# Performance work log

Measured on AMD Instinct MI355X. Metric: run time of the kernel, lower is better.

## Reference

```python
import jax, jax.numpy as jnp
import numpy as np

GROUP_SIZE = 64  # matches init_kwargs group_size


def setup_inputs() -> dict:
    key = jax.random.key(0)
    k1, k2, k3, k4 = jax.random.split(key, 4)
    B, S, D_in, D_out = 4, 2048, 4096, 4096
    x = jax.random.normal(k1, (B, S, D_in), dtype=jnp.float32)
    # symmetric int8 quantized weights in [-127, 127]
    weight_quant = jax.random.randint(k2, (D_out, D_in), -127, 128, dtype=jnp.int32)
    num_groups = (D_out * D_in) // GROUP_SIZE
    # positive per-group scales (abs_max / 127 of a typical weight group)
    weight_scale = jax.random.uniform(k3, (num_groups,), dtype=jnp.float32,
                                      minval=1e-3, maxval=2e-2)
    bias = jax.random.normal(k4, (D_out,), dtype=jnp.float32) * 0.01
    return {"x": x, "weight_quant": weight_quant,
            "weight_scale": weight_scale, "bias": bias}


def reference(x, weight_quant, weight_scale, bias):
    # Group-wise symmetric dequantization: flatten row-major, scale each
    # contiguous group of GROUP_SIZE elements by its own scale.
    out_f, in_f = weight_quant.shape
    w = weight_quant.astype(jnp.float32).reshape(-1, GROUP_SIZE)  # [num_groups, G]
    w = w * weight_scale[:, None]
    w = w.reshape(out_f, in_f).astype(x.dtype)
    # F.linear(x, W, b) = x @ W^T + b
    return jnp.einsum('bsi,oi->bso', x, w) + bias
```

## Files before the change

### kernel.cpp

```cpp
#include <hip/hip_runtime.h>
#include <stdint.h>


#define BM 128
#define BN 128
#define BK 64

typedef __attribute__((ext_vector_type(8))) short short8;
typedef __attribute__((ext_vector_type(8))) unsigned short ushort8;
typedef __attribute__((ext_vector_type(16))) float f32x16;
typedef __attribute__((ext_vector_type(4))) float float4v;
typedef __attribute__((ext_vector_type(4))) int int4v;

typedef __attribute__((address_space(1))) void g_void;
typedef __attribute__((address_space(3))) void l_void;

__device__ __forceinline__ unsigned short f2bf(float f) {
  union { float f; unsigned int u; } v; v.f = f;
  unsigned int r = v.u + 0x7FFFu + ((v.u >> 16) & 1u);
  return (unsigned short)(r >> 16);
}

__device__ __forceinline__ void async_copy16(const void* g, void* l) {
  __builtin_amdgcn_global_load_lds((const g_void*)g, (l_void*)l, 16, 0, 0);
}

__global__ __launch_bounds__(256) void cvt_kernel(
    const float* __restrict__ x, const int* __restrict__ w,
    const float* __restrict__ s, unsigned short* __restrict__ ox,
    unsigned short* __restrict__ ow, int n8x, int n8w, int gx) {
  if ((int)blockIdx.x < gx) {
    int t = blockIdx.x * 256 + threadIdx.x;
    if (t >= n8x) return;
    const float4v* xp = (const float4v*)x + (size_t)t * 2;
    float4v a = xp[0], b = xp[1];
    ushort8 r;
    r[0] = f2bf(a[0]); r[1] = f2bf(a[1]); r[2] = f2bf(a[2]); r[3] = f2bf(a[3]);
    r[4] = f2bf(b[0]); r[5] = f2bf(b[1]); r[6] = f2bf(b[2]); r[7] = f2bf(b[3]);
    *(ushort8*)(ox + (size_t)t * 8) = r;
  } else {
    int t = ((int)blockIdx.x - gx) * 256 + threadIdx.x;
    if (t >= n8w) return;
    const int4v* wp = (const int4v*)w + (size_t)t * 2;
    int4v q0 = wp[0], q1 = wp[1];
    float sc = s[t >> 3];
    ushort8 r;
    r[0] = f2bf((float)q0[0] * sc); r[1] = f2bf((float)q0[1] * sc);
    r[2] = f2bf((float)q0[2] * sc); r[3] = f2bf((float)q0[3] * sc);
    r[4] = f2bf((float)q1[0] * sc); r[5] = f2bf((float)q1[1] * sc);
    r[6] = f2bf((float)q1[2] * sc); r[7] = f2bf((float)q1[3] * sc);
    *(ushort8*)(ow + (size_t)t * 8) = r;
  }
}

__global__ __launch_bounds__(256, 4) void gemm_pre(
    const unsigned short* __restrict__ Xb,
    const unsigned short* __restrict__ Wb,
    const float* __restrict__ bias,
    float* __restrict__ C, int M, int N, int K) {
  __shared__ unsigned char smem[(BM * BK + BN * BK) * 2];
  const int tid = threadIdx.x;
  const int lane = tid & 63, wid = tid >> 6;
  const int m0 = blockIdx.y * BM, n0 = blockIdx.x * BN;

  const int sr = lane >> 3;
  const int fc = (lane & 7) ^ sr;
  const int offA = ((m0 + wid * 32 + sr) * K + fc * 8) * 2;
  const int offB = ((n0 + wid * 32 + sr) * K + fc * 8) * 2;
  const char* Xc = (const char*)Xb;
  const char* Wc = (const char*)Wb;

  unsigned char* As = smem;
  unsigned char* Bs = smem + BM * BK * 2;
  unsigned char* ldsA = As + wid * 4096;
  unsigned char* ldsB = Bs + wid * 4096;

  const int l31 = lane & 31, lh = lane >> 5, le = lane & 7;
  const int wm = (wid & 1) * 64, wn = (wid >> 1) * 64;
  const unsigned char* Aw = As + (wm + l31) * 128;
  const unsigned char* Bw = Bs + (wn + l31) * 128;

  f32x16 acc[2][2];
#pragma unroll
  for (int i = 0; i < 2; i++)
#pragma unroll
    for (int j = 0; j < 2; j++) acc[i][j] = (f32x16)(0.f);

  for (int k0 = 0; k0 < K; k0 += BK) {
    const int kb = k0 * 2;
#pragma unroll
    for (int t = 0; t < 4; t++) {
      async_copy16(Xc + (size_t)(offA + kb) + (size_t)t * (K * 16), ldsA + t * 1024);
      async_copy16(Wc + (size_t)(offB + kb) + (size_t)t * (K * 16), ldsB + t * 1024);
    }
    __syncthreads();

#pragma unroll
    for (int s = 0; s < 4; s++) {
      const int off = ((s + 4 * lh) ^ le) << 4;
      short8 a0 = *(const short8*)(Aw + off);
      short8 a1 = *(const short8*)(Aw + 4096 + off);
      short8 b0 = *(const short8*)(Bw + off);
      short8 b1 = *(const short8*)(Bw + 4096 + off);
      acc[0][0] = __builtin_amdgcn_mfma_f32_32x32x16_bf16(a0, b0, acc[0][0], 0, 0, 0);
      acc[0][1] = __builtin_amdgcn_mfma_f32_32x32x16_bf16(a0, b1, acc[0][1], 0, 0, 0);
      acc[1][0] = __builtin_amdgcn_mfma_f32_32x32x16_bf16(a1, b0, acc[1][0], 0, 0, 0);
      acc[1][1] = __builtin_amdgcn_mfma_f32_32x32x16_bf16(a1, b1, acc[1][1], 0, 0, 0);
    }
    __syncthreads();
  }

  const int gm = m0 + wm + 4 * lh, gn = n0 + wn + l31;
#pragma unroll
  for (int j = 0; j < 2; j++) {
    const int col = gn + j * 32;
    const float bv = bias[col];
#pragma unroll
    for (int i = 0; i < 2; i++) {
      const int rbase = gm + i * 32;
      f32x16 v = acc[i][j];
#pragma unroll
      for (int r = 0; r < 16; r++) {
        const int row = rbase + (r & 3) + 8 * (r >> 2);
        C[(size_t)row * N + col] = v[r] + bv;
      }
    }
  }
}

__global__ __launch_bounds__(256) void gemm_fused(
    const float* __restrict__ Xf, const int* __restrict__ Wq,
    const float* __restrict__ Ws, const float* __restrict__ bias,
    float* __restrict__ C, int M, int N, int K) {
  __shared__ unsigned char smem[(BM * BK + BN * BK) * 2];
  const int tid = threadIdx.x;
  const int lane = tid & 63, wid = tid >> 6;
  const int m0 = blockIdx.y * BM, n0 = blockIdx.x * BN;
  const int sr = lane >> 3, fc = (lane & 7) ^ sr;
  const int arow = m0 + wid * 32 + sr, brow = n0 + wid * 32 + sr;
  unsigned char* As = smem;
  unsigned char* Bs = smem + BM * BK * 2;
  unsigned char* stA = As + wid * 4096 + lane * 16;
  unsigned char* stB = Bs + wid * 4096 + lane * 16;
  const int l31 = lane & 31, lh = lane >> 5, le = lane & 7;
  const int wm = (wid & 1) * 64, wn = (wid >> 1) * 64;
  const unsigned char* Aw = As + (wm + l31) * 128;
  const unsigned char* Bw = Bs + (wn + l31) * 128;
  const int Kg = K >> 6;

  f32x16 acc[2][2];
#pragma unroll
  for (int i = 0; i < 2; i++)
#pragma unroll
    for (int j = 0; j < 2; j++) acc[i][j] = (f32x16)(0.f);

  for (int k0 = 0; k0 < K; k0 += BK) {
#pragma unroll
    for (int t = 0; t < 4; t++) {
      const float4v* xa = (const float4v*)(Xf + (size_t)(arow + t * 8) * K + k0 + fc * 8);
      float4v x0 = xa[0], x1 = xa[1];
      ushort8 ra;
      ra[0] = f2bf(x0[0]); ra[1] = f2bf(x0[1]); ra[2] = f2bf(x0[2]); ra[3] = f2bf(x0[3]);
      ra[4] = f2bf(x1[0]); ra[5] = f2bf(x1[1]); ra[6] = f2bf(x1[2]); ra[7] = f2bf(x1[3]);
      *(ushort8*)(stA + t * 1024) = ra;
      const int4v* wq = (const int4v*)(Wq + (size_t)(brow + t * 8) * K + k0 + fc * 8);
      int4v q0 = wq[0], q1 = wq[1];
      float sc = Ws[(size_t)(brow + t * 8) * Kg + (k0 >> 6)];
      ushort8 rb;
      rb[0] = f2bf((float)q0[0] * sc); rb[1] = f2bf((float)q0[1] * sc);
      rb[2] = f2bf((float)q0[2] * sc); rb[3] = f2bf((float)q0[3] * sc);
      rb[4] = f2bf((float)q1[0] * sc); rb[5] = f2bf((float)q1[1] * sc);
      rb[6] = f2bf((float)q1[2] * sc); rb[7] = f2bf((float)q1[3] * sc);
      *(ushort8*)(stB + t * 1024) = rb;
    }
    __syncthreads();
#pragma unroll
    for (int s = 0; s < 4; s++) {
      const int off = ((s + 4 * lh) ^ le) << 4;
      short8 a0 = *(const short8*)(Aw + off);
      short8 a1 = *(const short8*)(Aw + 4096 + off);
      short8 b0 = *(const short8*)(Bw + off);
      short8 b1 = *(const short8*)(Bw + 4096 + off);
      acc[0][0] = __builtin_amdgcn_mfma_f32_32x32x16_bf16(a0, b0, acc[0][0], 0, 0, 0);
      acc[0][1] = __builtin_amdgcn_mfma_f32_32x32x16_bf16(a0, b1, acc[0][1], 0, 0, 0);
      acc[1][0] = __builtin_amdgcn_mfma_f32_32x32x16_bf16(a1, b0, acc[1][0], 0, 0, 0);
      acc[1][1] = __builtin_amdgcn_mfma_f32_32x32x16_bf16(a1, b1, acc[1][1], 0, 0, 0);
    }
    __syncthreads();
  }

  const int gm = m0 + wm + 4 * lh, gn = n0 + wn + l31;
#pragma unroll
  for (int j = 0; j < 2; j++) {
    const int col = gn + j * 32;
    const float bv = bias[col];
#pragma unroll
    for (int i = 0; i < 2; i++) {
      const int rbase = gm + i * 32;
      f32x16 v = acc[i][j];
#pragma unroll
      for (int r = 0; r < 16; r++) {
        const int row = rbase + (r & 3) + 8 * (r >> 2);
        C[(size_t)row * N + col] = v[r] + bv;
      }
    }
  }
}

extern "C" void kernel_launch(void* const* d_in, const int* in_sizes, int n_in,
                              void* d_out, int out_size, void* d_ws, size_t ws_size,
                              hipStream_t stream) {
  const float* x = (const float*)d_in[0];
  const int* wq = (const int*)d_in[1];
  const float* wsc = (const float*)d_in[2];
  const float* bias = (const float*)d_in[3];
  float* out = (float*)d_out;

  const int N = in_sizes[3];
  const int K = in_sizes[1] / N;
  const int M = in_sizes[0] / K;

  const size_t needX = (size_t)M * K * 2;
  const size_t needW = (size_t)N * K * 2;
  dim3 grid(N / BN, M / BM), block(256);

  if (ws_size >= needX + needW) {
    unsigned short* Xb = (unsigned short*)d_ws;
    unsigned short* Wb = (unsigned short*)((char*)d_ws + needX);
    const int n8x = (M * K) / 8, n8w = (N * K) / 8;
    const int gx = (n8x + 255) / 256, gw = (n8w + 255) / 256;
    cvt_kernel<<<gx + gw, 256, 0, stream>>>(x, wq, wsc, Xb, Wb, n8x, n8w, gx);
    gemm_pre<<<grid, block, 0, stream>>>(Xb, Wb, bias, out, M, N, K);
  } else {
    gemm_fused<<<grid, block, 0, stream>>>(x, wq, wsc, bias, out, M, N, K);
  }
}
```

Measured before the change: 541.8 us.

## Replace bf16 GEMM with 256x256 double-buffered 8-wave pipelined kernel

Replaces the 128x128 single-buffered GEMM with a 256x256-tile, 512-thread kernel that double-buffers LDS (128 KB) and interleaves async global-to-LDS loads with 16x16x32 MFMA phases, using explicit vmcnt waits, raw barriers and s_setprio. It also remaps block IDs across 8 groups for L2 locality and gives each wave a 128x64 sub-tile for more register reuse. The aim is to hide memory latency behind compute and cut LDS and global traffic per FLOP. In exchange it uses much more LDS and registers, relies on a hand-tuned schedule, and only applies when shapes are multiples of 256.

```diff
diff --git a/kernel.cpp b/kernel.cpp
--- a/kernel.cpp
+++ b/kernel.cpp
@@ -2,12 +2,9 @@
 #include <stdint.h>
 
 
-#define BM 128
-#define BN 128
-#define BK 64
-
 typedef __attribute__((ext_vector_type(8))) short short8;
 typedef __attribute__((ext_vector_type(8))) unsigned short ushort8;
+typedef __attribute__((ext_vector_type(4))) float f32x4;
 typedef __attribute__((ext_vector_type(16))) float f32x16;
 typedef __attribute__((ext_vector_type(4))) float float4v;
 typedef __attribute__((ext_vector_type(4))) int int4v;
@@ -24,6 +21,14 @@
 __device__ __forceinline__ void async_copy16(const void* g, void* l) {
   __builtin_amdgcn_global_load_lds((const g_void*)g, (l_void*)l, 16, 0, 0);
 }
+
+__device__ __forceinline__ void wg_barrier() {
+  asm volatile("" ::: "memory");
+  __builtin_amdgcn_s_barrier();
+  asm volatile("" ::: "memory");
+}
+
+#define WAIT_VMCNT(N) asm volatile("s_waitcnt vmcnt(" #N ")" ::: "memory")
 
 __global__ __launch_bounds__(256) void cvt_kernel(
     const float* __restrict__ x, const int* __restrict__ w,
@@ -53,80 +58,176 @@
   }
 }
 
-__global__ __launch_bounds__(256, 4) void gemm_pre(
+
+#define MF(a, b, c) __builtin_amdgcn_mfma_f32_16x16x32_bf16(a, b, c, 0, 0, 0)
+
+#define LDA(base, mh) do {                              \
+    const unsigned char* _p = (base) + aoff + (mh) * 4096; \
+    av0 = *(const short8*)(_p);                         \
+    av1 = *(const short8*)(_p + 1024);                  \
+    av2 = *(const short8*)(_p + 2048);                  \
+    av3 = *(const short8*)(_p + 3072);                  \
+  } while (0)
+
+#define LDB(base) do {                                  \
+    const unsigned char* _p = (base) + boff;            \
+    bv0 = *(const short8*)(_p);                         \
+    bv1 = *(const short8*)(_p + 1024);                  \
+    bv2 = *(const short8*)(_p + 2048);                  \
+    bv3 = *(const short8*)(_p + 3072);                  \
+  } while (0)
+
+#define MM16(mb) do {                                           \
+    acc[(mb)+0][0] = MF(av0, bv0, acc[(mb)+0][0]);              \
+    acc[(mb)+0][1] = MF(av0, bv1, acc[(mb)+0][1]);              \
+    acc[(mb)+0][2] = MF(av0, bv2, acc[(mb)+0][2]);              \
+    acc[(mb)+0][3] = MF(av0, bv3, acc[(mb)+0][3]);              \
+    acc[(mb)+1][0] = MF(av1, bv0, acc[(mb)+1][0]);              \
+    acc[(mb)+1][1] = MF(av1, bv1, acc[(mb)+1][1]);              \
+    acc[(mb)+1][2] = MF(av1, bv2, acc[(mb)+1][2]);              \
+    acc[(mb)+1][3] = MF(av1, bv3, acc[(mb)+1][3]);              \
+    acc[(mb)+2][0] = MF(av2, bv0, acc[(mb)+2][0]);              \
+    acc[(mb)+2][1] = MF(av2, bv1, acc[(mb)+2][1]);              \
+    acc[(mb)+2][2] = MF(av2, bv2, acc[(mb)+2][2]);              \
+    acc[(mb)+2][3] = MF(av2, bv3, acc[(mb)+2][3]);              \
+    acc[(mb)+3][0] = MF(av3, bv0, acc[(mb)+3][0]);              \
+    acc[(mb)+3][1] = MF(av3, bv1, acc[(mb)+3][1]);              \
+    acc[(mb)+3][2] = MF(av3, bv2, acc[(mb)+3][2]);              \
+    acc[(mb)+3][3] = MF(av3, bv3, acc[(mb)+3][3]);              \
+  } while (0)
+
+#define PRIO1 __builtin_amdgcn_s_setprio(1)
+#define PRIO0 __builtin_amdgcn_s_setprio(0)
+
+__device__ __forceinline__ void stage2(const unsigned short* src, int rstride,
+                                       unsigned char* dst) {
+  async_copy16(src, dst);
+  async_copy16(src + rstride, dst + 8192);
+}
+
+__global__ __launch_bounds__(512, 2) void gemm_8p(
     const unsigned short* __restrict__ Xb,
     const unsigned short* __restrict__ Wb,
     const float* __restrict__ bias,
     float* __restrict__ C, int M, int N, int K) {
-  __shared__ unsigned char smem[(BM * BK + BN * BK) * 2];
+  __shared__ __align__(16) unsigned char smem[131072];
   const int tid = threadIdx.x;
-  const int lane = tid & 63, wid = tid >> 6;
-  const int m0 = blockIdx.y * BM, n0 = blockIdx.x * BN;
-
-  const int sr = lane >> 3;
-  const int fc = (lane & 7) ^ sr;
-  const int offA = ((m0 + wid * 32 + sr) * K + fc * 8) * 2;
-  const int offB = ((n0 + wid * 32 + sr) * K + fc * 8) * 2;
-  const char* Xc = (const char*)Xb;
-  const char* Wc = (const char*)Wb;
-
-  unsigned char* As = smem;
-  unsigned char* Bs = smem + BM * BK * 2;
-  unsigned char* ldsA = As + wid * 4096;
-  unsigned char* ldsB = Bs + wid * 4096;
-
-  const int l31 = lane & 31, lh = lane >> 5, le = lane & 7;
-  const int wm = (wid & 1) * 64, wn = (wid >> 1) * 64;
-  const unsigned char* Aw = As + (wm + l31) * 128;
-  const unsigned char* Bw = Bs + (wn + l31) * 128;
-
-  f32x16 acc[2][2];
-#pragma unroll
-  for (int i = 0; i < 2; i++)
-#pragma unroll
-    for (int j = 0; j < 2; j++) acc[i][j] = (f32x16)(0.f);
-
-  for (int k0 = 0; k0 < K; k0 += BK) {
-    const int kb = k0 * 2;
-#pragma unroll
-    for (int t = 0; t < 4; t++) {
-      async_copy16(Xc + (size_t)(offA + kb) + (size_t)t * (K * 16), ldsA + t * 1024);
-      async_copy16(Wc + (size_t)(offB + kb) + (size_t)t * (K * 16), ldsB + t * 1024);
+  const int lane = tid & 63, w = tid >> 6;
+  const int wm = w >> 2, wn = w & 3;
+  const int l15 = lane & 15;
+
+  const int nbn = N >> 8;
+  int bid = blockIdx.x;
+  {
+    const int nwg = gridDim.x;
+    if ((nwg & 7) == 0) bid = (bid & 7) * (nwg >> 3) + (bid >> 3);
+  }
+  const int m0 = (bid / nbn) << 8;
+  const int n0 = (bid % nbn) << 8;
+
+  const int chnk = (((lane >> 4) ^ ((l15 >> 1) & 3)) << 4);
+  const int aoff = (wm * 128 + l15) * 64 + chnk;
+  const int boff = (wn * 64 + l15) * 64 + chnk;
+
+  const int rl = tid >> 2;
+  const int lc = (tid & 3) ^ ((tid >> 3) & 3);
+  const unsigned short* pA = Xb + (size_t)(m0 + rl) * K + lc * 8;
+  const unsigned short* pB = Wb + (size_t)(n0 + rl) * K + lc * 8;
+  const int rstride = K << 7;
+  const int wuo = w << 10;
+
+  f32x4 acc[8][4];
+#pragma unroll
+  for (int i = 0; i < 8; i++)
+#pragma unroll
+    for (int j = 0; j < 4; j++) acc[i][j] = (f32x4)(0.f);
+
+  const int NT = K >> 6;
+
+  stage2(pA, rstride, smem + wuo);
+  stage2(pB, rstride, smem + 65536 + wuo);
+  stage2(pA + 32, rstride, smem + 16384 + wuo);
+  stage2(pB + 32, rstride, smem + 65536 + 16384 + wuo);
+  WAIT_VMCNT(4);
+  wg_barrier();
+
+  short8 av0, av1, av2, av3, bv0, bv1, bv2, bv3;
+
+  for (int t = 0; t < NT - 1; ++t) {
+    const int p = t & 1;
+    const unsigned char* Ab = smem + p * 32768;
+    const unsigned char* Bb = smem + 65536 + p * 32768;
+    unsigned char* Aq = smem + (p ^ 1) * 32768 + wuo;
+    unsigned char* Bq = smem + 65536 + (p ^ 1) * 32768 + wuo;
+    const unsigned short* sA = pA + (size_t)(t + 1) * 64;
+    const unsigned short* sB = pB + (size_t)(t + 1) * 64;
+
+    LDA(Ab, 0); LDB(Bb);
+    stage2(sA, rstride, Aq);
+    wg_barrier();
+    PRIO1; MM16(0); PRIO0;
+    wg_barrier();
+    LDA(Ab, 1);
+    stage2(sB, rstride, Bq);
+    wg_barrier();
+    PRIO1; MM16(4); PRIO0;
+    WAIT_VMCNT(4);
+    wg_barrier();
+    LDA(Ab + 16384, 0); LDB(Bb + 16384);
+    stage2(sA + 32, rstride, Aq + 16384);
+    wg_barrier();
+    PRIO1; MM16(0); PRIO0;
+    wg_barrier();
+    LDA(Ab + 16384, 1);
+    stage2(sB + 32, rstride, Bq + 16384);
+    wg_barrier();
+    PRIO1; MM16(4); PRIO0;
+    WAIT_VMCNT(4);
+    wg_barrier();
+  }
+
+  {
+    const int p = (NT - 1) & 1;
+    const unsigned char* Ab = smem + p * 32768;
+    const unsigned char* Bb = smem + 65536 + p * 32768;
+    LDA(Ab, 0); LDB(Bb);
+    wg_barrier();
+    PRIO1; MM16(0); PRIO0;
+    wg_barrier();
+    LDA(Ab, 1);
+    wg_barrier();
+    PRIO1; MM16(4); PRIO0;
+    WAIT_VMCNT(0);
+    wg_barrier();
+    LDA(Ab + 16384, 0); LDB(Bb + 16384);
+    wg_barrier();
+    PRIO1; MM16(0); PRIO0;
+    wg_barrier();
+    LDA(Ab + 16384, 1);
+    wg_barrier();
+    PRIO1; MM16(4); PRIO0;
+  }
+
+  const int gm = m0 + wm * 128 + ((lane >> 4) << 2);
+  const int gn = n0 + wn * 64 + l15;
+  float bvs[4];
+#pragma unroll
+  for (int g = 0; g < 4; ++g) bvs[g] = bias[gn + g * 16];
+#pragma unroll
+  for (int mf = 0; mf < 8; ++mf) {
+    const size_t rb = (size_t)(gm + mf * 16) * N + gn;
+#pragma unroll
+    for (int r = 0; r < 4; ++r) {
+#pragma unroll
+      for (int g = 0; g < 4; ++g)
+        C[rb + (size_t)r * N + g * 16] = acc[mf][g][r] + bvs[g];
     }
-    __syncthreads();
-
-#pragma unroll
-    for (int s = 0; s < 4; s++) {
-      const int off = ((s + 4 * lh) ^ le) << 4;
-      short8 a0 = *(const short8*)(Aw + off);
-      short8 a1 = *(const short8*)(Aw + 4096 + off);
-      short8 b0 = *(const short8*)(Bw + off);
-      short8 b1 = *(const short8*)(Bw + 4096 + off);
-      acc[0][0] = __builtin_amdgcn_mfma_f32_32x32x16_bf16(a0, b0, acc[0][0], 0, 0, 0);
-      acc[0][1] = __builtin_amdgcn_mfma_f32_32x32x16_bf16(a0, b1, acc[0][1], 0, 0, 0);
-      acc[1][0] = __builtin_amdgcn_mfma_f32_32x32x16_bf16(a1, b0, acc[1][0], 0, 0, 0);
-      acc[1][1] = __builtin_amdgcn_mfma_f32_32x32x16_bf16(a1, b1, acc[1][1], 0, 0, 0);
-    }
-    __syncthreads();
-  }
-
-  const int gm = m0 + wm + 4 * lh, gn = n0 + wn + l31;
-#pragma unroll
-  for (int j = 0; j < 2; j++) {
-    const int col = gn + j * 32;
-    const float bv = bias[col];
-#pragma unroll
-    for (int i = 0; i < 2; i++) {
-      const int rbase = gm + i * 32;
-      f32x16 v = acc[i][j];
-#pragma unroll
-      for (int r = 0; r < 16; r++) {
-        const int row = rbase + (r & 3) + 8 * (r >> 2);
-        C[(size_t)row * N + col] = v[r] + bv;
-      }
-    }
-  }
-}
+  }
+}
+
+#define BM 128
+#define BN 128
+#define BK 64
 
 __global__ __launch_bounds__(256) void gemm_fused(
     const float* __restrict__ Xf, const int* __restrict__ Wq,
@@ -222,16 +323,18 @@
 
   const size_t needX = (size_t)M * K * 2;
   const size_t needW = (size_t)N * K * 2;
-  dim3 grid(N / BN, M / BM), block(256);
-
-  if (ws_size >= needX + needW) {
+  const bool big = (M % 256 == 0) && (N % 256 == 0) && (K % 64 == 0) && (K >= 128);
+
+  if (big && ws_size >= needX + needW) {
     unsigned short* Xb = (unsigned short*)d_ws;
     unsigned short* Wb = (unsigned short*)((char*)d_ws + needX);
     const int n8x = (M * K) / 8, n8w = (N * K) / 8;
     const int gx = (n8x + 255) / 256, gw = (n8w + 255) / 256;
     cvt_kernel<<<gx + gw, 256, 0, stream>>>(x, wq, wsc, Xb, Wb, n8x, n8w, gx);
-    gemm_pre<<<grid, block, 0, stream>>>(Xb, Wb, bias, out, M, N, K);
+    dim3 grid((M / 256) * (N / 256));
+    gemm_8p<<<grid, 512, 0, stream>>>(Xb, Wb, bias, out, M, N, K);
   } else {
+    dim3 grid(N / BN, M / BM), block(256);
     gemm_fused<<<grid, block, 0, stream>>>(x, wq, wsc, bias, out, M, N, K);
   }
 }
```

New measurement: 500.6 us. -7.6%, faster.
